# Kernel optimization log

Measured on AMD Instinct MI355X. Metric: run time of the kernel, lower is better.

Reference implementation:

```python
import jax, jax.numpy as jnp
import numpy as np

H, W, CIN, COUT, B = 56, 56, 64, 64, 32
K = 3            # kernel_size
WIN = 15         # win_range
R = (WIN - 1) // 2


def _make_sample_idx():
    """Per-pixel fixed random sample locations within a WINxWIN window,
    mirroring Dconv_drop.__init__ (random.sample over valid window indices)."""
    rng = np.random.default_rng(0)
    ii = np.arange(H)[:, None, None]          # [H,1,1]
    jj = np.arange(W)[None, :, None]          # [1,W,1]
    lo_i = np.maximum(0, ii - R); hi_i = np.minimum(H - 1, ii + R)
    lo_j = np.maximum(0, jj - R); hi_j = np.minimum(W - 1, jj + R)
    ri = rng.integers(np.broadcast_to(lo_i, (H, W, K * K)),
                      np.broadcast_to(hi_i, (H, W, K * K)) + 1)
    rj = rng.integers(np.broadcast_to(lo_j, (H, W, K * K)),
                      np.broadcast_to(hi_j, (H, W, K * K)) + 1)
    return (ri * W + rj).astype(np.int32)    # [H,W,9] indices into H*W


def setup_inputs() -> dict:
    key = jax.random.key(0)
    k1, k2 = jax.random.split(key)
    x = jax.random.normal(k1, (B, CIN, H, W), dtype=jnp.float32)
    weight = jax.random.normal(k2, (COUT, CIN, K, K), dtype=jnp.float32) * 0.05
    sample_idx = jnp.asarray(_make_sample_idx())
    return {"x": x, "weight": weight, "sample_idx": sample_idx}


def reference(x, weight, sample_idx):
    # x: [B,C,H,W]; sample_idx: [H,W,9] flat indices into H*W.
    # Original: scatter gathered pixels into [B,C,3H,3W] grid, then
    # stride-3 kernel-3 conv => per-pixel contraction over the 9 samples.
    b, c, h, w = x.shape
    x_flat = x.reshape(b, c, h * w)
    gathered = x_flat[:, :, sample_idx]              # [B,C,H,W,9]
    w_flat = weight.reshape(weight.shape[0], c, K * K)  # [O,C,9]
    out = jnp.einsum('bchwk,ock->bohw', gathered, w_flat)
    return out
```

## Files before the change

kernel.cpp:

```cpp
#include <hip/hip_runtime.h>
#include <hip/hip_bf16.h>

#define HH 56
#define WW 56
#define CIN 64
#define COUT 64
#define BATCH 32
#define KK 9
#define HWP (HH*WW)
#define NS 18
#define NTILE 49
#define NBLK (NTILE*BATCH)
#define XT_OFF 73728
#define XSW 33

typedef __attribute__((ext_vector_type(8))) short short8;
typedef __attribute__((ext_vector_type(4))) float float4v;
typedef __attribute__((ext_vector_type(4))) unsigned int uint4v;

__device__ __forceinline__ unsigned short f2bf(float f) {
    union { float f; unsigned u; } v; v.f = f;
    unsigned r = v.u + 0x7FFFu + ((v.u >> 16) & 1u);
    return (unsigned short)(r >> 16);
}

__device__ __forceinline__ void prepack_elem(const float* __restrict__ w,
                                             unsigned short* __restrict__ apack,
                                             int e) {
    int j = e & 7;
    int l = (e >> 3) & 63;
    int ss = e >> 9;
    int mb = ss / 18;
    int s  = ss - mb * 18;
    int o = mb * 16 + (l & 15);
    int c = ((s & 1) << 5) + ((l >> 4) << 3) + j;
    int k = s >> 1;
    apack[e] = f2bf(w[(o * CIN + c) * KK + k]);
}

__global__ __launch_bounds__(256) void prep_kernel(
    const float* __restrict__ x, const float* __restrict__ w,
    unsigned int* __restrict__ xt, unsigned short* __restrict__ apack)
{
    int bid = blockIdx.x;
    int t   = threadIdx.x;
    if (bid < 784) {
        int u   = bid * 256 + t;
        int c2q = u & 7;
        int hq  = u >> 3;
        int b   = hq / 784;
        int q   = hq - b * 784;
        int hw  = q * 4;
        const float* xb = x + ((size_t)b * CIN + c2q * 8) * HWP + hw;
        float4v f[8];
        #pragma unroll
        for (int i = 0; i < 8; ++i)
            f[i] = *(const float4v*)(xb + (size_t)i * HWP);
        unsigned int* xto = xt + ((size_t)b * HWP + hw) * 32 + c2q * 4;
        #pragma unroll
        for (int j = 0; j < 4; ++j) {
            uint4v o;
            #pragma unroll
            for (int ci = 0; ci < 4; ++ci)
                o[ci] = (unsigned)f2bf(f[2 * ci][j]) |
                        ((unsigned)f2bf(f[2 * ci + 1][j]) << 16);
            *(uint4v*)(xto + (size_t)j * 32) = o;
        }
    } else {
        prepack_elem(w, apack, (bid - 784) * 256 + t);
    }
}

__global__ __launch_bounds__(256) void prep_weights_only(
    const float* __restrict__ w, unsigned short* __restrict__ apack)
{
    prepack_elem(w, apack, blockIdx.x * 256 + threadIdx.x);
}

__global__ __launch_bounds__(256) void dconv_main(
    const unsigned int* __restrict__ xt, const int* __restrict__ sidx,
    const unsigned short* __restrict__ apack, float* __restrict__ out)
{
    __shared__ unsigned int xs[496 * 16];

    const int t    = threadIdx.x;
    const int lane = t & 63;
    const int wv   = t >> 6;
    const int col  = lane & 15;
    const int krow = lane >> 4;

    int bid  = blockIdx.x;
    int orig = (bid & 7) * 196 + (bid >> 3);
    int b    = orig / NTILE;
    int bx   = orig - b * NTILE;
    int ti = bx / 7, tj = bx - (bx / 7) * 7;
    int r0 = ti * 8 - 7; if (r0 < 0) r0 = 0;
    int c0 = tj * 8 - 7; if (c0 < 0) c0 = 0;

    const unsigned int* xtb = xt + (size_t)b * HWP * 32;

    int lb[4][KK];
    #pragma unroll
    for (int nn = 0; nn < 4; ++nn) {
        int p  = nn * 16 + col;
        int gi = ti * 8 + (p >> 3), gj = tj * 8 + (p & 7);
        const int* sp = sidx + (gi * WW + gj) * KK;
        #pragma unroll
        for (int k = 0; k < KK; ++k) {
            int g  = sp[k];
            int si = g / WW, sj = g - si * WW;
            int row = (si - r0) * 22 + (sj - c0);
            lb[nn][k] = row * 64 + ((krow ^ (row & 3)) << 4);
        }
    }

    const unsigned short* apW = apack + (size_t)(wv * NS) * 512 + lane * 8;

    float4v zero = {0.f, 0.f, 0.f, 0.f};
    float4v acc[4] = {zero, zero, zero, zero};
    const char* xsb = (const char*)xs;

    #pragma unroll
    for (int sh = 0; sh < 2; ++sh) {
        for (int grp = wv; grp < 31; grp += 4) {
            int row = grp * 16 + (lane >> 2);
            int rc  = row < 483 ? row : 483;
            int lsr = rc / 22;
            int lsc = rc - lsr * 22;
            int si = r0 + lsr; if (si > HH - 1) si = HH - 1;
            int sj = c0 + lsc; if (sj > WW - 1) sj = WW - 1;
            int q  = (lane & 3) ^ (rc & 3);
            const unsigned int* src =
                xtb + (size_t)(si * WW + sj) * 32 + sh * 16 + (q << 2);
            __builtin_amdgcn_global_load_lds(
                (const __attribute__((address_space(1))) unsigned int*)src,
                (__attribute__((address_space(3))) unsigned int*)(xs + grp * 256),
                16, 0, 0);
        }
        __syncthreads();

        #pragma unroll
        for (int k = 0; k < KK; ++k) {
            short8 a = *(const short8*)(apW + (size_t)(2 * k + sh) * 512);
            #pragma unroll
            for (int nn = 0; nn < 4; ++nn) {
                short8 bv = *(const short8*)(xsb + lb[nn][k]);
                acc[nn] = __builtin_amdgcn_mfma_f32_16x16x32_bf16(
                    a, bv, acc[nn], 0, 0, 0);
            }
        }
        if (sh == 0) __syncthreads();
    }

    float* ob = out + ((size_t)b * COUT + wv * 16) * HWP;
    #pragma unroll
    for (int nn = 0; nn < 4; ++nn) {
        int p = nn * 16 + col;
        int g = (ti * 8 + (p >> 3)) * WW + tj * 8 + (p & 7);
        #pragma unroll
        for (int r = 0; r < 4; ++r)
            ob[(krow * 4 + r) * HWP + g] = acc[nn][r];
    }
}

__global__ __launch_bounds__(256, 2) void dconv_fb(
    const float* __restrict__ x, const int* __restrict__ sidx,
    const unsigned short* __restrict__ apack, float* __restrict__ out)
{
    __shared__ unsigned int xs[484 * XSW];

    const int t    = threadIdx.x;
    const int lane = t & 63;
    const int wv   = t >> 6;
    const int mbp  = wv >> 1;
    const int ntp  = wv & 1;
    const int col  = lane & 15;
    const int krow = lane >> 4;
    const int bx   = blockIdx.x;
    const int b    = blockIdx.y;
    const int ti = bx / 7, tj = bx - (bx / 7) * 7;
    int r0 = ti * 8 - 7; if (r0 < 0) r0 = 0;
    int r1 = ti * 8 + 14; if (r1 > HH - 1) r1 = HH - 1;
    int c0 = tj * 8 - 7; if (c0 < 0) c0 = 0;
    int c1 = tj * 8 + 14; if (c1 > WW - 1) c1 = WW - 1;

    int lb[2][KK];
    #pragma unroll
    for (int nn = 0; nn < 2; ++nn) {
        int p  = (ntp * 2 + nn) * 16 + col;
        int gi = ti * 8 + (p >> 3), gj = tj * 8 + (p & 7);
        const int* sp = sidx + (gi * WW + gj) * KK;
        #pragma unroll
        for (int k = 0; k < KK; ++k) {
            int g  = sp[k];
            int si = g / WW, sj = g - si * WW;
            lb[nn][k] = ((si - r0) * 22 + (sj - c0)) * (XSW * 4);
        }
    }

    short8 areg[2][NS];
    #pragma unroll
    for (int m = 0; m < 2; ++m) {
        const unsigned short* ap = apack + ((mbp * 2 + m) * NS) * 512 + lane * 8;
        #pragma unroll
        for (int s = 0; s < NS; ++s)
            areg[m][s] = *(const short8*)(ap + s * 512);
    }

    const float* xb = x + (size_t)b * CIN * HWP;
    for (int e = t; e < 32 * 512; e += 256) {
        int c2 = e >> 9, ls = e & 511;
        if (ls < 484) {
            int lsr = ls / 22;
            int si = r0 + lsr, sj = c0 + (ls - lsr * 22);
            if (si <= r1 && sj <= c1) {
                int g = si * WW + sj;
                float f0 = xb[(2 * c2) * HWP + g];
                float f1 = xb[(2 * c2 + 1) * HWP + g];
                xs[ls * XSW + c2] =
                    (unsigned)f2bf(f0) | ((unsigned)f2bf(f1) << 16);
            }
        }
    }
    __syncthreads();

    float4v zero = {0.f, 0.f, 0.f, 0.f};
    float4v acc[2][2] = {{zero, zero}, {zero, zero}};
    const char* xsb = (const char*)xs + krow * 16;

    #pragma unroll
    for (int k = 0; k < KK; ++k) {
        #pragma unroll
        for (int nn = 0; nn < 2; ++nn) {
            const char* ba = xsb + lb[nn][k];
            union { int i[4]; short8 s8; } b0, b1;
            #pragma unroll
            for (int w = 0; w < 4; ++w) {
                b0.i[w] = *(const int*)(ba + w * 4);
                b1.i[w] = *(const int*)(ba + 64 + w * 4);
            }
            acc[0][nn] = __builtin_amdgcn_mfma_f32_16x16x32_bf16(
                areg[0][2 * k], b0.s8, acc[0][nn], 0, 0, 0);
            acc[1][nn] = __builtin_amdgcn_mfma_f32_16x16x32_bf16(
                areg[1][2 * k], b0.s8, acc[1][nn], 0, 0, 0);
            acc[0][nn] = __builtin_amdgcn_mfma_f32_16x16x32_bf16(
                areg[0][2 * k + 1], b1.s8, acc[0][nn], 0, 0, 0);
            acc[1][nn] = __builtin_amdgcn_mfma_f32_16x16x32_bf16(
                areg[1][2 * k + 1], b1.s8, acc[1][nn], 0, 0, 0);
        }
    }

    float* ob = out + ((size_t)b * COUT + mbp * 32) * HWP;
    #pragma unroll
    for (int m = 0; m < 2; ++m) {
        #pragma unroll
        for (int nn = 0; nn < 2; ++nn) {
            int p = (ntp * 2 + nn) * 16 + col;
            int g = (ti * 8 + (p >> 3)) * WW + tj * 8 + (p & 7);
            #pragma unroll
            for (int r = 0; r < 4; ++r)
                ob[(m * 16 + krow * 4 + r) * HWP + g] = acc[m][nn][r];
        }
    }
}

extern "C" void kernel_launch(void* const* d_in, const int* in_sizes, int n_in,
                              void* d_out, int out_size, void* d_ws, size_t ws_size,
                              hipStream_t stream) {
    const float* x    = (const float*)d_in[0];
    const float* w    = (const float*)d_in[1];
    const int*   sidx = (const int*)d_in[2];
    float* out = (float*)d_out;
    unsigned short* apack = (unsigned short*)d_ws;
    unsigned int*   xt    = (unsigned int*)((char*)d_ws + XT_OFF);

    size_t need = (size_t)XT_OFF + (size_t)BATCH * HWP * 128;
    if (ws_size >= need) {
        prep_kernel<<<928, 256, 0, stream>>>(x, w, xt, apack);
        dconv_main<<<NBLK, 256, 0, stream>>>(xt, sidx, apack, out);
    } else {
        prep_weights_only<<<144, 256, 0, stream>>>(w, apack);
        dim3 grid(NTILE, BATCH);
        dconv_fb<<<grid, 256, 0, stream>>>(x, sidx, apack, out);
    }
}
```

Measured before the change: 35.12 us.

## Process two batches per block with double-buffered LDS staging

Each block now handles two batch images for the same spatial tile, which halves the grid and reuses the sample-index offsets and the precomputed source addresses across both images. LDS is doubled into two buffers so that staging of the next image or channel half overlaps the MFMA compute on the current one. Weight fragments are preloaded into registers per channel half and reused for both images. This raises register and LDS use per block, and the launch bound now asks for two blocks per CU. Fewer blocks also means less parallelism to spread across the CUs.

```diff
diff --git a/kernel.cpp b/kernel.cpp
--- a/kernel.cpp
+++ b/kernel.cpp
@@ -10,9 +10,10 @@
 #define HWP (HH*WW)
 #define NS 18
 #define NTILE 49
-#define NBLK (NTILE*BATCH)
+#define NBLK2 784
 #define XT_OFF 73728
 #define XSW 33
+#define BUFW 7936
 
 typedef __attribute__((ext_vector_type(8))) short short8;
 typedef __attribute__((ext_vector_type(4))) float float4v;
@@ -77,11 +78,11 @@
     prepack_elem(w, apack, blockIdx.x * 256 + threadIdx.x);
 }
 
-__global__ __launch_bounds__(256) void dconv_main(
+__global__ __launch_bounds__(256, 2) void dconv_main(
     const unsigned int* __restrict__ xt, const int* __restrict__ sidx,
     const unsigned short* __restrict__ apack, float* __restrict__ out)
 {
-    __shared__ unsigned int xs[496 * 16];
+    __shared__ unsigned int xs[2 * BUFW];
 
     const int t    = threadIdx.x;
     const int lane = t & 63;
@@ -90,14 +91,28 @@
     const int krow = lane >> 4;
 
     int bid  = blockIdx.x;
-    int orig = (bid & 7) * 196 + (bid >> 3);
-    int b    = orig / NTILE;
-    int bx   = orig - b * NTILE;
+    int orig = (bid & 7) * 98 + (bid >> 3);
+    int bp   = orig / NTILE;
+    int bx   = orig - bp * NTILE;
+    int b0   = bp * 2;
     int ti = bx / 7, tj = bx - (bx / 7) * 7;
     int r0 = ti * 8 - 7; if (r0 < 0) r0 = 0;
     int c0 = tj * 8 - 7; if (c0 < 0) c0 = 0;
 
-    const unsigned int* xtb = xt + (size_t)b * HWP * 32;
+    const unsigned int* xtb0 = xt + (size_t)b0 * HWP * 32;
+
+    int pixq[8];
+    #pragma unroll
+    for (int it = 0; it < 8; ++it) {
+        int grp = wv + it * 4;
+        int row = grp * 16 + (lane >> 2);
+        int rc  = row < 483 ? row : 483;
+        int lsr = rc / 22;
+        int lsc = rc - lsr * 22;
+        int si = r0 + lsr; if (si > HH - 1) si = HH - 1;
+        int sj = c0 + lsc; if (sj > WW - 1) sj = WW - 1;
+        pixq[it] = (si * WW + sj) * 32 + (((lane & 3) ^ (rc & 3)) << 2);
+    }
 
     int lb[4][KK];
     #pragma unroll
@@ -117,49 +132,83 @@
     const unsigned short* apW = apack + (size_t)(wv * NS) * 512 + lane * 8;
 
     float4v zero = {0.f, 0.f, 0.f, 0.f};
-    float4v acc[4] = {zero, zero, zero, zero};
-    const char* xsb = (const char*)xs;
-
-    #pragma unroll
-    for (int sh = 0; sh < 2; ++sh) {
-        for (int grp = wv; grp < 31; grp += 4) {
-            int row = grp * 16 + (lane >> 2);
-            int rc  = row < 483 ? row : 483;
-            int lsr = rc / 22;
-            int lsc = rc - lsr * 22;
-            int si = r0 + lsr; if (si > HH - 1) si = HH - 1;
-            int sj = c0 + lsc; if (sj > WW - 1) sj = WW - 1;
-            int q  = (lane & 3) ^ (rc & 3);
-            const unsigned int* src =
-                xtb + (size_t)(si * WW + sj) * 32 + sh * 16 + (q << 2);
-            __builtin_amdgcn_global_load_lds(
-                (const __attribute__((address_space(1))) unsigned int*)src,
-                (__attribute__((address_space(3))) unsigned int*)(xs + grp * 256),
-                16, 0, 0);
-        }
-        __syncthreads();
-
-        #pragma unroll
-        for (int k = 0; k < KK; ++k) {
-            short8 a = *(const short8*)(apW + (size_t)(2 * k + sh) * 512);
+    float4v acc[2][4];
+    #pragma unroll
+    for (int ba = 0; ba < 2; ++ba)
+        #pragma unroll
+        for (int nn = 0; nn < 4; ++nn) acc[ba][nn] = zero;
+
+#define STAGE(BA, SH, BUF)                                                     \
+    {                                                                          \
+        _Pragma("unroll")                                                      \
+        for (int it = 0; it < 8; ++it) {                                       \
+            int grp = wv + it * 4;                                             \
+            if (grp < 31) {                                                    \
+                const unsigned int* src =                                      \
+                    xtb0 + (size_t)(BA) * HWP * 32 + pixq[it] + (SH) * 16;     \
+                __builtin_amdgcn_global_load_lds(                              \
+                    (const __attribute__((address_space(1))) unsigned int*)src,\
+                    (__attribute__((address_space(3))) unsigned int*)          \
+                        (xs + (BUF) * BUFW + grp * 256),                       \
+                    16, 0, 0);                                                 \
+            }                                                                  \
+        }                                                                      \
+    }
+
+#define COMPUTE(BA, AR, BUF)                                                   \
+    {                                                                          \
+        const char* bufB = (const char*)(xs + (BUF) * BUFW);                   \
+        _Pragma("unroll")                                                      \
+        for (int k = 0; k < KK; ++k) {                                         \
+            _Pragma("unroll")                                                  \
+            for (int nn = 0; nn < 4; ++nn) {                                   \
+                short8 bv = *(const short8*)(bufB + lb[nn][k]);                \
+                acc[BA][nn] = __builtin_amdgcn_mfma_f32_16x16x32_bf16(         \
+                    AR[k], bv, acc[BA][nn], 0, 0, 0);                          \
+            }                                                                  \
+        }                                                                      \
+    }
+
+    short8 aR0[KK];
+    #pragma unroll
+    for (int k = 0; k < KK; ++k)
+        aR0[k] = *(const short8*)(apW + (size_t)(2 * k) * 512);
+
+    STAGE(0, 0, 0);
+    __syncthreads();
+
+    STAGE(1, 0, 1);
+    COMPUTE(0, aR0, 0);
+    __syncthreads();
+
+    STAGE(0, 1, 0);
+    short8 aR1[KK];
+    #pragma unroll
+    for (int k = 0; k < KK; ++k)
+        aR1[k] = *(const short8*)(apW + (size_t)(2 * k + 1) * 512);
+    COMPUTE(1, aR0, 1);
+    __syncthreads();
+
+    STAGE(1, 1, 1);
+    COMPUTE(0, aR1, 0);
+    __syncthreads();
+
+    COMPUTE(1, aR1, 1);
+
+#undef STAGE
+#undef COMPUTE
+
+    #pragma unroll
+    for (int ba = 0; ba < 2; ++ba) {
+        float* ob = out + ((size_t)(b0 + ba) * COUT + wv * 16) * HWP;
+        #pragma unroll
+        for (int nn = 0; nn < 4; ++nn) {
+            int p = nn * 16 + col;
+            int g = (ti * 8 + (p >> 3)) * WW + tj * 8 + (p & 7);
             #pragma unroll
-            for (int nn = 0; nn < 4; ++nn) {
-                short8 bv = *(const short8*)(xsb + lb[nn][k]);
-                acc[nn] = __builtin_amdgcn_mfma_f32_16x16x32_bf16(
-                    a, bv, acc[nn], 0, 0, 0);
-            }
-        }
-        if (sh == 0) __syncthreads();
-    }
-
-    float* ob = out + ((size_t)b * COUT + wv * 16) * HWP;
-    #pragma unroll
-    for (int nn = 0; nn < 4; ++nn) {
-        int p = nn * 16 + col;
-        int g = (ti * 8 + (p >> 3)) * WW + tj * 8 + (p & 7);
-        #pragma unroll
-        for (int r = 0; r < 4; ++r)
-            ob[(krow * 4 + r) * HWP + g] = acc[nn][r];
+            for (int r = 0; r < 4; ++r)
+                ob[(krow * 4 + r) * HWP + g] = acc[ba][nn][r];
+        }
     }
 }
 
@@ -277,7 +326,7 @@
     size_t need = (size_t)XT_OFF + (size_t)BATCH * HWP * 128;
     if (ws_size >= need) {
         prep_kernel<<<928, 256, 0, stream>>>(x, w, xt, apack);
-        dconv_main<<<NBLK, 256, 0, stream>>>(xt, sidx, apack, out);
+        dconv_main<<<NBLK2, 256, 0, stream>>>(xt, sidx, apack, out);
     } else {
         prep_weights_only<<<144, 256, 0, stream>>>(w, apack);
         dim3 grid(NTILE, BATCH);
```

Result: slower. 38.11 us (+8.5%).
